# Kernel tuning notes

Hardware: AMD Instinct MI355X
Metric: run time of the kernel (lower is better)

Reference implementation:

```python
import jax, jax.numpy as jnp
import numpy as np

H = 1024      # hidden_size
I = 2048      # expert intermediate_size (SwiGLU)
E = 8         # num_local_experts
B, S = 2, 4096
EPS = 1e-5
INIT = 0.02


def setup_inputs() -> dict:
    key = jax.random.key(0)
    ks = jax.random.split(key, 9)
    return {
        "hidden_states": jax.random.normal(ks[0], (B, S, H), jnp.float32),
        "ln_w": jnp.ones((H,), jnp.float32),
        "ln_b": jnp.zeros((H,), jnp.float32),
        "router_w": jax.random.normal(ks[1], (H, E), jnp.float32) * INIT,
        "gate_w": jax.random.normal(ks[2], (E, H, I), jnp.float32) * INIT,
        "up_w": jax.random.normal(ks[3], (E, H, I), jnp.float32) * INIT,
        "down_w": jax.random.normal(ks[4], (E, I, H), jnp.float32) * INIT,
        "sh_gate": jax.random.normal(ks[5], (H, I), jnp.float32) * INIT,
        "sh_up": jax.random.normal(ks[6], (H, I), jnp.float32) * INIT,
        "sh_down": jax.random.normal(ks[7], (I, H), jnp.float32) * INIT,
    }


def _layernorm(x, w, b):
    mu = jnp.mean(x, axis=-1, keepdims=True)
    var = jnp.mean(jnp.square(x - mu), axis=-1, keepdims=True)
    return (x - mu) * jax.lax.rsqrt(var + EPS) * w + b


def reference(hidden_states, ln_w, ln_b, router_w, gate_w, up_w, down_w,
              sh_gate, sh_up, sh_down):
    b, s, h = hidden_states.shape
    normed = _layernorm(hidden_states, ln_w, ln_b)
    xf = normed.reshape(-1, h)                       # [T, H]

    # Router: top-1 expert per token, sigmoid gating (Llama-4 style)
    logits = xf @ router_w                           # [T, E]
    top_idx = jnp.argmax(logits, axis=-1)            # [T]
    top_score = jax.nn.sigmoid(jnp.max(logits, axis=-1))  # [T]

    # Routed experts: scan over experts, mask+scale tokens assigned to each.
    def body(acc, ew):
        g, u, d, e = ew
        w = jnp.where(top_idx == e, top_score, 0.0)[:, None]  # [T, 1]
        xe = xf * w                                            # gate score applied to input
        hmid = jax.nn.silu(xe @ g) * (xe @ u)                  # [T, I]
        return acc + hmid @ d, None

    routed, _ = jax.lax.scan(
        body, jnp.zeros_like(xf), (gate_w, up_w, down_w, jnp.arange(E)))

    # Shared expert (dense SwiGLU) applied to all tokens
    shared = (jax.nn.silu(xf @ sh_gate) * (xf @ sh_up)) @ sh_down  # [T, H]

    moe_out = (routed + shared).reshape(b, s, h)
    return hidden_states + moe_out
```

## Files before the change

kernel.cpp:

```cpp
#include <hip/hip_runtime.h>

typedef unsigned short ushort_t;
typedef unsigned int uint_t;

#define T_TOK 8192
#define HDIM 1024
#define IDIM 2048
#define NEXP 8
#define RPAD_MAX 10240
#define TOTROWS (RPAD_MAX + T_TOK)

using f32x4 = __attribute__((ext_vector_type(4))) float;
using s16x8 = __attribute__((ext_vector_type(8))) short;

#define SBAR() do { asm volatile("" ::: "memory"); __builtin_amdgcn_s_barrier(); asm volatile("" ::: "memory"); } while (0)
#define VMW(n) asm volatile("s_waitcnt vmcnt(" #n ")" ::: "memory")
#define LGKM(n) do { asm volatile("s_waitcnt lgkmcnt(" #n ")" ::: "memory"); __builtin_amdgcn_sched_barrier(0); } while (0)

__device__ __forceinline__ float b2f(ushort_t h) {
    return __uint_as_float(((uint_t)h) << 16);
}
__device__ __forceinline__ ushort_t f2bf(float f) {
    uint_t u = __float_as_uint(f);
    uint_t r = (u + 0x7FFFu + ((u >> 16) & 1u)) >> 16;
    return (ushort_t)r;
}
__device__ __forceinline__ void gload16(const void* g, void* l) {
    __builtin_amdgcn_global_load_lds(
        (const __attribute__((address_space(1))) void*)g,
        (__attribute__((address_space(3))) void*)l, 16, 0, 0);
}
__device__ __forceinline__ void gdec(int gi, int& r, int& kg) {
    int prow = gi >> 3, v = (gi & 7) ^ (prow & 7);
    r = 2 * prow + (v >> 2);
    kg = v & 3;
}

__global__ void tcvt_gu(const float* __restrict__ gw, const float* __restrict__ shg,
                        const float* __restrict__ uw, const float* __restrict__ shu,
                        ushort_t* __restrict__ gwt, ushort_t* __restrict__ uwt) {
    __shared__ float tile[32][33];
    int z = blockIdx.z, zz = z % 9;
    const float* src;
    ushort_t* dst;
    if (z < 9) {
        src = zz < 8 ? gw + (size_t)zz * HDIM * IDIM : shg;
        dst = gwt + (size_t)zz * IDIM * HDIM;
    } else {
        src = zz < 8 ? uw + (size_t)zz * HDIM * IDIM : shu;
        dst = uwt + (size_t)zz * IDIM * HDIM;
    }
    int c0 = blockIdx.x * 32, r0 = blockIdx.y * 32;
    int tx = threadIdx.x, ty = threadIdx.y;
#pragma unroll
    for (int i = 0; i < 32; i += 8)
        tile[ty + i][tx] = src[(size_t)(r0 + ty + i) * IDIM + c0 + tx];
    __syncthreads();
#pragma unroll
    for (int i = 0; i < 32; i += 8)
        dst[(size_t)(c0 + ty + i) * HDIM + r0 + tx] = f2bf(tile[tx][ty + i]);
}
__global__ void tcvt_d(const float* __restrict__ dw, const float* __restrict__ shd,
                       ushort_t* __restrict__ dwt) {
    __shared__ float tile[32][33];
    int z = blockIdx.z;
    const float* src = z < 8 ? dw + (size_t)z * IDIM * HDIM : shd;
    ushort_t* dst = dwt + (size_t)z * HDIM * IDIM;
    int c0 = blockIdx.x * 32, r0 = blockIdx.y * 32;
    int tx = threadIdx.x, ty = threadIdx.y;
#pragma unroll
    for (int i = 0; i < 32; i += 8)
        tile[ty + i][tx] = src[(size_t)(r0 + ty + i) * HDIM + c0 + tx];
    __syncthreads();
#pragma unroll
    for (int i = 0; i < 32; i += 8)
        dst[(size_t)(c0 + ty + i) * IDIM + r0 + tx] = f2bf(tile[tx][ty + i]);
}

__global__ void ln_router(const float* __restrict__ x, const float* __restrict__ lnw,
                          const float* __restrict__ lnb, const float* __restrict__ rw,
                          ushort_t* __restrict__ normed, int* __restrict__ top_idx,
                          float* __restrict__ top_score, int* __restrict__ cnt) {
    int t = blockIdx.x, tid = threadIdx.x;
    const float* xr = x + (size_t)t * HDIM;
    float v[4];
    float s = 0.f, ss = 0.f;
#pragma unroll
    for (int i = 0; i < 4; i++) {
        v[i] = xr[tid + i * 256];
        s += v[i];
        ss += v[i] * v[i];
    }
#pragma unroll
    for (int o = 32; o; o >>= 1) {
        s += __shfl_down(s, o);
        ss += __shfl_down(ss, o);
    }
    __shared__ float rs_[4], rss_[4], stats[2];
    int wid = tid >> 6, lane = tid & 63;
    if (!lane) { rs_[wid] = s; rss_[wid] = ss; }
    __syncthreads();
    if (!tid) {
        float S = rs_[0] + rs_[1] + rs_[2] + rs_[3];
        float SS = rss_[0] + rss_[1] + rss_[2] + rss_[3];
        float mu = S * (1.f / HDIM);
        float var = SS * (1.f / HDIM) - mu * mu;
        stats[0] = mu;
        stats[1] = rsqrtf(var + 1e-5f);
    }
    __syncthreads();
    float mu = stats[0], rsg = stats[1];
    float lg[8] = {0, 0, 0, 0, 0, 0, 0, 0};
#pragma unroll
    for (int i = 0; i < 4; i++) {
        int h = tid + i * 256;
        float xn = (v[i] - mu) * rsg * lnw[h] + lnb[h];
        normed[(size_t)t * HDIM + h] = f2bf(xn);
        const float* rwh = rw + (size_t)h * NEXP;
#pragma unroll
        for (int e = 0; e < 8; e++) lg[e] += xn * rwh[e];
    }
#pragma unroll
    for (int o = 32; o; o >>= 1)
#pragma unroll
        for (int e = 0; e < 8; e++) lg[e] += __shfl_down(lg[e], o);
    __shared__ float lred[4][8];
    if (!lane)
#pragma unroll
        for (int e = 0; e < 8; e++) lred[wid][e] = lg[e];
    __syncthreads();
    if (!tid) {
        float best = -1e30f;
        int bi = 0;
#pragma unroll
        for (int e = 0; e < 8; e++) {
            float L = lred[0][e] + lred[1][e] + lred[2][e] + lred[3][e];
            if (L > best) { best = L; bi = e; }
        }
        top_idx[t] = bi;
        top_score[t] = 1.f / (1.f + __expf(-best));
        atomicAdd(&cnt[bi], 1);
    }
}

__global__ void scan_k(const int* __restrict__ cnt, int* __restrict__ pad_off,
                       int* __restrict__ fill) {
    if (threadIdx.x == 0) {
        int o = 0;
        for (int e = 0; e < NEXP; e++) {
            pad_off[e] = o;
            o += (cnt[e] + 255) & ~255;
        }
        pad_off[NEXP] = o;
    }
    if (threadIdx.x < NEXP) fill[threadIdx.x] = 0;
}

__global__ void scatter_k(const ushort_t* __restrict__ normed, const int* __restrict__ top_idx,
                          const float* __restrict__ top_score, const int* __restrict__ pad_off,
                          int* __restrict__ fill, int* __restrict__ order,
                          ushort_t* __restrict__ xs) {
    int t = blockIdx.x, tid = threadIdx.x;
    __shared__ int spos;
    if (!tid) {
        int e = top_idx[t];
        int p = pad_off[e] + atomicAdd(&fill[e], 1);
        order[p] = t;
        spos = p;
    }
    __syncthreads();
    int pos = spos;
    float sc = top_score[t];
    const ushort4* src = (const ushort4*)(normed + (size_t)t * HDIM);
    ushort4* dst = (ushort4*)(xs + (size_t)pos * HDIM);
    ushort4 a = src[tid];
    a.x = f2bf(b2f(a.x) * sc);
    a.y = f2bf(b2f(a.y) * sc);
    a.z = f2bf(b2f(a.z) * sc);
    a.w = f2bf(b2f(a.w) * sc);
    dst[tid] = a;
}

__global__ __launch_bounds__(512, 2) void gemm1_k(
    const ushort_t* __restrict__ X, const ushort_t* __restrict__ Wg,
    const ushort_t* __restrict__ Wu, const int* __restrict__ pad_off,
    ushort_t* __restrict__ hmid) {
    __shared__ __align__(16) ushort_t lds[4 * 16384];
    const int RT = TOTROWS / 256, CT = IDIM / 128;
    const int NH = HDIM / 32;
    int nwg = RT * CT;
    int bid = blockIdx.x;
    int q = nwg >> 3, r = nwg & 7;
    int xcd = bid & 7, idx = bid >> 3;
    int wg = (xcd < r ? xcd * (q + 1) : r * (q + 1) + (xcd - r) * q) + idx;
    int rt = wg / CT, ct = wg % CT;
    int row0 = rt * 256, col0 = ct * 128;
    int e;
    if (row0 >= RPAD_MAX) e = 8;
    else {
        if (row0 >= pad_off[NEXP]) return;
        e = 0;
        while (row0 >= pad_off[e + 1]) ++e;
    }
    const ushort_t* wgp = Wg + (size_t)e * IDIM * HDIM;
    const ushort_t* wup = Wu + (size_t)e * IDIM * HDIM;

    const int tid = threadIdx.x, l = tid & 63, w = tid >> 6;
    const int wm = w >> 2, wn = w & 3;
    const int lr = l & 15, lg4 = l >> 4;

    int rA0, kA0, rA1, kA1, rB, kB;
    gdec(tid, rA0, kA0);
    gdec(512 + tid, rA1, kA1);
    gdec(tid, rB, kB);
    const ushort_t* srcA0 = X + (size_t)(row0 + rA0) * HDIM + kA0 * 8;
    const ushort_t* srcA1 = X + (size_t)(row0 + rA1) * HDIM + kA1 * 8;
    const ushort_t* srcBg = wgp + (size_t)(col0 + rB) * HDIM + kB * 8;
    const ushort_t* srcBu = wup + (size_t)(col0 + rB) * HDIM + kB * 8;
    const int dA0 = tid * 8, dA1 = (512 + tid) * 8, dB = tid * 8;

    const int s_slot = (((l & 1) << 2) | lg4) ^ ((l >> 1) & 7);
    const int aoff = (wm * 64 + (lr >> 1)) * 64 + s_slot * 8;
    const int boff = (wn * 16 + (lr >> 1)) * 64 + s_slot * 8;

    f32x4 accg[8][2] = {};
    f32x4 accu[8][2] = {};

#define G1_STAGE(h) do { int ko = (h) * 32; int hb_ = ((h) & 3) * 16384;       \
        gload16(srcA0 + ko, &lds[hb_ + dA0]);                                  \
        gload16(srcA1 + ko, &lds[hb_ + dA1]);                                  \
        gload16(srcBg + ko, &lds[hb_ + 8192 + dB]);                            \
        gload16(srcBu + ko, &lds[hb_ + 12288 + dB]); } while (0)

#define G1_PH(h, VMWAIT, DOSTAGE) do {                                         \
        const int hb = ((h) & 3) * 16384;                                      \
        s16x8 av[8], bv[4];                                                    \
        _Pragma("unroll")                                                      \
        for (int i = 0; i < 4; ++i) av[i] = *(const s16x8*)&lds[hb + aoff + i * 512]; \
        _Pragma("unroll")                                                      \
        for (int i = 0; i < 2; ++i) bv[i] = *(const s16x8*)&lds[hb + 8192 + boff + i * 512]; \
        _Pragma("unroll")                                                      \
        for (int i = 0; i < 2; ++i) bv[2 + i] = *(const s16x8*)&lds[hb + 12288 + boff + i * 512]; \
        _Pragma("unroll")                                                      \
        for (int i = 0; i < 4; ++i) av[4 + i] = *(const s16x8*)&lds[hb + aoff + 2048 + i * 512]; \
        if (DOSTAGE) G1_STAGE((h) + 3);                                        \
        VMWAIT;                                                                \
        SBAR();                                                                \
        LGKM(4);                                                               \
        __builtin_amdgcn_s_setprio(1);                                         \
        _Pragma("unroll")                                                      \
        for (int m = 0; m < 4; ++m) {                                          \
            accg[m][0] = __builtin_amdgcn_mfma_f32_16x16x32_bf16(av[m], bv[0], accg[m][0], 0, 0, 0); \
            accg[m][1] = __builtin_amdgcn_mfma_f32_16x16x32_bf16(av[m], bv[1], accg[m][1], 0, 0, 0); \
            accu[m][0] = __builtin_amdgcn_mfma_f32_16x16x32_bf16(av[m], bv[2], accu[m][0], 0, 0, 0); \
            accu[m][1] = __builtin_amdgcn_mfma_f32_16x16x32_bf16(av[m], bv[3], accu[m][1], 0, 0, 0); \
        }                                                                      \
        __builtin_amdgcn_s_setprio(0);                                         \
        LGKM(0);                                                               \
        __builtin_amdgcn_s_setprio(1);                                         \
        _Pragma("unroll")                                                      \
        for (int m = 0; m < 4; ++m) {                                          \
            accg[4 + m][0] = __builtin_amdgcn_mfma_f32_16x16x32_bf16(av[4 + m], bv[0], accg[4 + m][0], 0, 0, 0); \
            accg[4 + m][1] = __builtin_amdgcn_mfma_f32_16x16x32_bf16(av[4 + m], bv[1], accg[4 + m][1], 0, 0, 0); \
            accu[4 + m][0] = __builtin_amdgcn_mfma_f32_16x16x32_bf16(av[4 + m], bv[2], accu[4 + m][0], 0, 0, 0); \
            accu[4 + m][1] = __builtin_amdgcn_mfma_f32_16x16x32_bf16(av[4 + m], bv[3], accu[4 + m][1], 0, 0, 0); \
        }                                                                      \
        __builtin_amdgcn_s_setprio(0);                                         \
        SBAR();                                                                \
    } while (0)

    G1_STAGE(0);
    G1_STAGE(1);
    G1_STAGE(2);
    VMW(8);
    SBAR();
    for (int h = 0; h < NH - 3; ++h) G1_PH(h, VMW(8), 1);
    G1_PH(NH - 3, VMW(4), 0);
    G1_PH(NH - 2, VMW(0), 0);
    G1_PH(NH - 1, VMW(0), 0);

#pragma unroll
    for (int mf = 0; mf < 8; ++mf) {
        int row = row0 + wm * 128 + mf * 16 + lg4 * 4;
#pragma unroll
        for (int nf = 0; nf < 2; ++nf) {
            int col = col0 + wn * 32 + nf * 16 + lr;
#pragma unroll
            for (int rr = 0; rr < 4; ++rr) {
                float g = accg[mf][nf][rr], u = accu[mf][nf][rr];
                float val = g / (1.f + __expf(-g)) * u;
                hmid[(size_t)(row + rr) * IDIM + col] = f2bf(val);
            }
        }
    }
#undef G1_STAGE
#undef G1_PH
}

template <int SHARED>
__global__ __launch_bounds__(512, 2) void gemm2_k(
    const ushort_t* __restrict__ Hm, const ushort_t* __restrict__ Wd,
    const int* __restrict__ pad_off, const int* __restrict__ order,
    const float* __restrict__ hs, float* __restrict__ out, int RT) {
    __shared__ __align__(16) ushort_t lds[4 * 12288];
    const int CT = HDIM / 128;
    const int NH = IDIM / 32;
    int nwg = RT * CT;
    int bid = blockIdx.x;
    int q = nwg >> 3, r = nwg & 7;
    int xcd = bid & 7, idx = bid >> 3;
    int wg = (xcd < r ? xcd * (q + 1) : r * (q + 1) + (xcd - r) * q) + idx;
    int rt = wg / CT, ct = wg % CT;
    int row0 = rt * 256, col0 = ct * 128;
    const ushort_t* wdp;
    if (SHARED) {
        wdp = Wd + (size_t)8 * HDIM * IDIM;
    } else {
        if (row0 >= pad_off[NEXP]) return;
        int e = 0;
        while (row0 >= pad_off[e + 1]) ++e;
        wdp = Wd + (size_t)e * HDIM * IDIM;
    }
    const int tid = threadIdx.x, l = tid & 63, w = tid >> 6;
    const int wm = w >> 1, wn = w & 1;
    const int lr = l & 15, lg4 = l >> 4;

    int rA0, kA0, rA1, kA1, rB, kB;
    gdec(tid, rA0, kA0);
    gdec(512 + tid, rA1, kA1);
    gdec(tid, rB, kB);
    const ushort_t* srcA0 = Hm + (size_t)(row0 + rA0) * IDIM + kA0 * 8;
    const ushort_t* srcA1 = Hm + (size_t)(row0 + rA1) * IDIM + kA1 * 8;
    const ushort_t* srcB = wdp + (size_t)(col0 + rB) * IDIM + kB * 8;
    const int dA0 = tid * 8, dA1 = (512 + tid) * 8, dB = tid * 8;

    const int s_slot = (((l & 1) << 2) | lg4) ^ ((l >> 1) & 7);
    const int aoff = (wm * 32 + (lr >> 1)) * 64 + s_slot * 8;
    const int boff = (wn * 32 + (lr >> 1)) * 64 + s_slot * 8;

    f32x4 acc[4][4] = {};

#define G2_STAGE(h) do { int ko = (h) * 32; int hb_ = ((h) & 3) * 12288;       \
        gload16(srcA0 + ko, &lds[hb_ + dA0]);                                  \
        gload16(srcA1 + ko, &lds[hb_ + dA1]);                                  \
        gload16(srcB + ko, &lds[hb_ + 8192 + dB]); } while (0)

#define G2_PH(h, VMWAIT, DOSTAGE) do {                                         \
        const int hb = ((h) & 3) * 12288;                                      \
        s16x8 av[4], bv[4];                                                    \
        _Pragma("unroll")                                                      \
        for (int i = 0; i < 4; ++i) av[i] = *(const s16x8*)&lds[hb + aoff + i * 512]; \
        _Pragma("unroll")                                                      \
        for (int i = 0; i < 4; ++i) bv[i] = *(const s16x8*)&lds[hb + 8192 + boff + i * 512]; \
        if (DOSTAGE) G2_STAGE((h) + 3);                                        \
        VMWAIT;                                                                \
        SBAR();                                                                \
        LGKM(0);                                                               \
        __builtin_amdgcn_s_setprio(1);                                         \
        _Pragma("unroll")                                                      \
        for (int m = 0; m < 4; ++m)                                            \
            _Pragma("unroll")                                                  \
            for (int n = 0; n < 4; ++n)                                        \
                acc[m][n] = __builtin_amdgcn_mfma_f32_16x16x32_bf16(av[m], bv[n], acc[m][n], 0, 0, 0); \
        __builtin_amdgcn_s_setprio(0);                                         \
        SBAR();                                                                \
    } while (0)

    G2_STAGE(0);
    G2_STAGE(1);
    G2_STAGE(2);
    VMW(6);
    SBAR();
    for (int h = 0; h < NH - 3; ++h) G2_PH(h, VMW(6), 1);
    G2_PH(NH - 3, VMW(3), 0);
    G2_PH(NH - 2, VMW(0), 0);
    G2_PH(NH - 1, VMW(0), 0);

#pragma unroll
    for (int mf = 0; mf < 4; ++mf) {
        int row = row0 + wm * 64 + mf * 16 + lg4 * 4;
#pragma unroll
        for (int nf = 0; nf < 4; ++nf) {
            int col = col0 + wn * 64 + nf * 16 + lr;
#pragma unroll
            for (int rr = 0; rr < 4; ++rr) {
                int rw_ = row + rr;
                if (SHARED) {
                    size_t o = (size_t)rw_ * HDIM + col;
                    out[o] += hs[o] + acc[mf][nf][rr];
                } else {
                    int tok = order[rw_];
                    if (tok >= 0) {
                        size_t o = (size_t)tok * HDIM + col;
                        out[o] = acc[mf][nf][rr];
                    }
                }
            }
        }
    }
#undef G2_STAGE
#undef G2_PH
}

extern "C" void kernel_launch(void* const* d_in, const int* in_sizes, int n_in,
                              void* d_out, int out_size, void* d_ws, size_t ws_size,
                              hipStream_t stream) {
    const float* hs = (const float*)d_in[0];
    const float* lnw = (const float*)d_in[1];
    const float* lnb = (const float*)d_in[2];
    const float* rw = (const float*)d_in[3];
    const float* gw = (const float*)d_in[4];
    const float* uw = (const float*)d_in[5];
    const float* dw = (const float*)d_in[6];
    const float* shg = (const float*)d_in[7];
    const float* shu = (const float*)d_in[8];
    const float* shd = (const float*)d_in[9];
    float* out = (float*)d_out;

    char* p = (char*)d_ws;
    auto alloc = [&](size_t bytes) {
        void* r = (void*)p;
        p += (bytes + 255) & ~(size_t)255;
        return r;
    };
    ushort_t* xsbuf = (ushort_t*)alloc((size_t)TOTROWS * HDIM * 2);
    ushort_t* hmid = (ushort_t*)alloc((size_t)TOTROWS * IDIM * 2);
    ushort_t* gwt = (ushort_t*)alloc((size_t)9 * IDIM * HDIM * 2);
    ushort_t* uwt = (ushort_t*)alloc((size_t)9 * IDIM * HDIM * 2);
    ushort_t* dwt = (ushort_t*)alloc((size_t)9 * HDIM * IDIM * 2);
    int* cnt = (int*)alloc(NEXP * 4);
    int* pad_off = (int*)alloc((NEXP + 1) * 4);
    int* fill = (int*)alloc(NEXP * 4);
    int* top_idx = (int*)alloc(T_TOK * 4);
    float* top_sc = (float*)alloc(T_TOK * 4);
    int* order = (int*)alloc(RPAD_MAX * 4);

    ushort_t* normed = xsbuf + (size_t)RPAD_MAX * HDIM;

    hipMemsetAsync(cnt, 0, NEXP * 4, stream);
    hipMemsetAsync(order, 0xFF, RPAD_MAX * 4, stream);
    hipMemsetAsync(xsbuf, 0, (size_t)RPAD_MAX * HDIM * 2, stream);

    dim3 tb(32, 8);
    tcvt_gu<<<dim3(IDIM / 32, HDIM / 32, 18), tb, 0, stream>>>(gw, shg, uw, shu, gwt, uwt);
    tcvt_d<<<dim3(HDIM / 32, IDIM / 32, 9), tb, 0, stream>>>(dw, shd, dwt);

    ln_router<<<T_TOK, 256, 0, stream>>>(hs, lnw, lnb, rw, normed, top_idx, top_sc, cnt);
    scan_k<<<1, 64, 0, stream>>>(cnt, pad_off, fill);
    scatter_k<<<T_TOK, 256, 0, stream>>>(normed, top_idx, top_sc, pad_off, fill, order, xsbuf);

    {
        int RT = TOTROWS / 256, CT = IDIM / 128;
        gemm1_k<<<RT * CT, 512, 0, stream>>>(xsbuf, gwt, uwt, pad_off, hmid);
    }
    {
        int RT = RPAD_MAX / 256;
        gemm2_k<0><<<RT * (HDIM / 128), 512, 0, stream>>>(
            hmid, dwt, pad_off, order, hs, out, RT);
    }
    {
        int RT = T_TOK / 256;
        gemm2_k<1><<<RT * (HDIM / 128), 512, 0, stream>>>(
            hmid + (size_t)RPAD_MAX * IDIM, dwt, pad_off, order, hs, out, RT);
    }
}
```

Baseline: 588.3 us.

## Merge weight transpose kernels into 64x64 tiles and add supertile block mapping

Replaces the two 32x32 transpose/convert kernels with one 64x64-tile kernel covering gate, up and down weights, writing 4-element bf16 vectors to cut launch count and narrow stores. Both grouped GEMMs now map block IDs onto 4x8 supertiles per XCD, so neighbouring workgroups on one XCD share A rows and B columns in its L2 cache. The expert search loop is also bounded at 7. The supertile mapping adds index arithmetic and assumes particular grid divisibility; the transpose reads LDS columns with possible bank conflicts.

```diff
diff --git a/kernel.cpp b/kernel.cpp
--- a/kernel.cpp
+++ b/kernel.cpp
@@ -35,46 +35,62 @@
     r = 2 * prow + (v >> 2);
     kg = v & 3;
 }
-
-__global__ void tcvt_gu(const float* __restrict__ gw, const float* __restrict__ shg,
-                        const float* __restrict__ uw, const float* __restrict__ shu,
-                        ushort_t* __restrict__ gwt, ushort_t* __restrict__ uwt) {
-    __shared__ float tile[32][33];
-    int z = blockIdx.z, zz = z % 9;
+__device__ __forceinline__ void sbmap(int bid, int SBC, int NSB, int& rt, int& ct) {
+    int x = bid & 7, j = bid >> 3;
+    int r = j >> 5, pos = j & 31;
+    int sb = r * 8 + x;
+    int rem = NSB - r * 8;
+    if (rem < 8) {
+        int share = 8 / rem;
+        int cap = 32 / share;
+        sb = r * 8 + x / share;
+        pos = (x % share) * cap + (pos % cap);
+    }
+    int sbr = sb / SBC, sbc = sb % SBC;
+    rt = sbr * 4 + (pos >> 3);
+    ct = sbc * 8 + (pos & 7);
+}
+
+__global__ void tcvt64(const float* __restrict__ gw, const float* __restrict__ shg,
+                       const float* __restrict__ uw, const float* __restrict__ shu,
+                       const float* __restrict__ dw, const float* __restrict__ shd,
+                       ushort_t* __restrict__ gwt, ushort_t* __restrict__ uwt,
+                       ushort_t* __restrict__ dwt) {
+    __shared__ float tile[64][65];
+    int z = blockIdx.z;
     const float* src;
     ushort_t* dst;
-    if (z < 9) {
-        src = zz < 8 ? gw + (size_t)zz * HDIM * IDIM : shg;
-        dst = gwt + (size_t)zz * IDIM * HDIM;
+    int R, C, bx = blockIdx.x, by = blockIdx.y;
+    if (z < 18) {
+        int zz = z % 9;
+        R = HDIM; C = IDIM;
+        if (z < 9) { src = zz < 8 ? gw + (size_t)zz * HDIM * IDIM : shg; dst = gwt + (size_t)zz * IDIM * HDIM; }
+        else       { src = zz < 8 ? uw + (size_t)zz * HDIM * IDIM : shu; dst = uwt + (size_t)zz * IDIM * HDIM; }
     } else {
-        src = zz < 8 ? uw + (size_t)zz * HDIM * IDIM : shu;
-        dst = uwt + (size_t)zz * IDIM * HDIM;
-    }
-    int c0 = blockIdx.x * 32, r0 = blockIdx.y * 32;
+        int zz = z - 18;
+        R = IDIM; C = HDIM;
+        src = zz < 8 ? dw + (size_t)zz * IDIM * HDIM : shd;
+        dst = dwt + (size_t)zz * HDIM * IDIM;
+        int t = bx; bx = by; by = t;
+    }
+    int c0 = bx * 64, r0 = by * 64;
     int tx = threadIdx.x, ty = threadIdx.y;
 #pragma unroll
-    for (int i = 0; i < 32; i += 8)
-        tile[ty + i][tx] = src[(size_t)(r0 + ty + i) * IDIM + c0 + tx];
+    for (int i = 0; i < 16; ++i)
+        tile[ty + i * 4][tx] = src[(size_t)(r0 + ty + i * 4) * C + c0 + tx];
     __syncthreads();
-#pragma unroll
-    for (int i = 0; i < 32; i += 8)
-        dst[(size_t)(c0 + ty + i) * HDIM + r0 + tx] = f2bf(tile[tx][ty + i]);
-}
-__global__ void tcvt_d(const float* __restrict__ dw, const float* __restrict__ shd,
-                       ushort_t* __restrict__ dwt) {
-    __shared__ float tile[32][33];
-    int z = blockIdx.z;
-    const float* src = z < 8 ? dw + (size_t)z * IDIM * HDIM : shd;
-    ushort_t* dst = dwt + (size_t)z * HDIM * IDIM;
-    int c0 = blockIdx.x * 32, r0 = blockIdx.y * 32;
-    int tx = threadIdx.x, ty = threadIdx.y;
-#pragma unroll
-    for (int i = 0; i < 32; i += 8)
-        tile[ty + i][tx] = src[(size_t)(r0 + ty + i) * HDIM + c0 + tx];
-    __syncthreads();
-#pragma unroll
-    for (int i = 0; i < 32; i += 8)
-        dst[(size_t)(c0 + ty + i) * IDIM + r0 + tx] = f2bf(tile[tx][ty + i]);
+    int tid = ty * 64 + tx;
+    int rr = (tid & 15) * 4, cc0 = tid >> 4;
+#pragma unroll
+    for (int it = 0; it < 4; ++it) {
+        int c = cc0 + it * 16;
+        ushort4 v;
+        v.x = f2bf(tile[rr + 0][c]);
+        v.y = f2bf(tile[rr + 1][c]);
+        v.z = f2bf(tile[rr + 2][c]);
+        v.w = f2bf(tile[rr + 3][c]);
+        *(ushort4*)&dst[(size_t)(c0 + c) * R + r0 + rr] = v;
+    }
 }
 
 __global__ void ln_router(const float* __restrict__ x, const float* __restrict__ lnw,
@@ -186,21 +202,17 @@
     const ushort_t* __restrict__ Wu, const int* __restrict__ pad_off,
     ushort_t* __restrict__ hmid) {
     __shared__ __align__(16) ushort_t lds[4 * 16384];
-    const int RT = TOTROWS / 256, CT = IDIM / 128;
+    const int CT = IDIM / 128;
     const int NH = HDIM / 32;
-    int nwg = RT * CT;
-    int bid = blockIdx.x;
-    int q = nwg >> 3, r = nwg & 7;
-    int xcd = bid & 7, idx = bid >> 3;
-    int wg = (xcd < r ? xcd * (q + 1) : r * (q + 1) + (xcd - r) * q) + idx;
-    int rt = wg / CT, ct = wg % CT;
+    int rt, ct;
+    sbmap(blockIdx.x, CT / 8, (TOTROWS / 256 / 4) * (CT / 8), rt, ct);
     int row0 = rt * 256, col0 = ct * 128;
     int e;
     if (row0 >= RPAD_MAX) e = 8;
     else {
         if (row0 >= pad_off[NEXP]) return;
         e = 0;
-        while (row0 >= pad_off[e + 1]) ++e;
+        while (e < 7 && row0 >= pad_off[e + 1]) ++e;
     }
     const ushort_t* wgp = Wg + (size_t)e * IDIM * HDIM;
     const ushort_t* wup = Wu + (size_t)e * IDIM * HDIM;
@@ -305,12 +317,8 @@
     __shared__ __align__(16) ushort_t lds[4 * 12288];
     const int CT = HDIM / 128;
     const int NH = IDIM / 32;
-    int nwg = RT * CT;
-    int bid = blockIdx.x;
-    int q = nwg >> 3, r = nwg & 7;
-    int xcd = bid & 7, idx = bid >> 3;
-    int wg = (xcd < r ? xcd * (q + 1) : r * (q + 1) + (xcd - r) * q) + idx;
-    int rt = wg / CT, ct = wg % CT;
+    int rt, ct;
+    sbmap(blockIdx.x, 1, RT / 4, rt, ct);
     int row0 = rt * 256, col0 = ct * 128;
     const ushort_t* wdp;
     if (SHARED) {
@@ -318,7 +326,7 @@
     } else {
         if (row0 >= pad_off[NEXP]) return;
         int e = 0;
-        while (row0 >= pad_off[e + 1]) ++e;
+        while (e < 7 && row0 >= pad_off[e + 1]) ++e;
         wdp = Wd + (size_t)e * HDIM * IDIM;
     }
     const int tid = threadIdx.x, l = tid & 63, w = tid >> 6;
@@ -441,9 +449,8 @@
     hipMemsetAsync(order, 0xFF, RPAD_MAX * 4, stream);
     hipMemsetAsync(xsbuf, 0, (size_t)RPAD_MAX * HDIM * 2, stream);
 
-    dim3 tb(32, 8);
-    tcvt_gu<<<dim3(IDIM / 32, HDIM / 32, 18), tb, 0, stream>>>(gw, shg, uw, shu, gwt, uwt);
-    tcvt_d<<<dim3(HDIM / 32, IDIM / 32, 9), tb, 0, stream>>>(dw, shd, dwt);
+    tcvt64<<<dim3(IDIM / 64, HDIM / 64, 27), dim3(64, 4), 0, stream>>>(
+        gw, shg, uw, shu, dw, shd, gwt, uwt, dwt);
 
     ln_router<<<T_TOK, 256, 0, stream>>>(hs, lnw, lnb, rw, normed, top_idx, top_sc, cnt);
     scan_k<<<1, 64, 0, stream>>>(cnt, pad_off, fill);
```

Measured after the change: 577.6 us. No clear change (-1.8%).
